# Optimization experiments

Hardware: AMD Instinct MI355X
Metric: run time of the kernel (lower is better)

The kernel has to match this reference:

```python
import jax, jax.numpy as jnp
import numpy as np

B, T, C, HS = 512, 256, 384, 64

def setup_inputs() -> dict:
    key = jax.random.key(0)
    kx, kq, kk, kv = jax.random.split(key, 4)
    x = jax.random.normal(kx, (B, T, C), dtype=jnp.float32)
    Wq = jax.random.normal(kq, (C, HS), dtype=jnp.float32) * (C ** -0.5)
    Wk = jax.random.normal(kk, (C, HS), dtype=jnp.float32) * (C ** -0.5)
    Wv = jax.random.normal(kv, (C, HS), dtype=jnp.float32) * (C ** -0.5)
    return {"x": x, "Wq": Wq, "Wk": Wk, "Wv": Wv}

def reference(x, Wq, Wk, Wv):
    # single-head causal self-attention (dropout = identity in eval mode)
    q = jnp.einsum('btc,ch->bth', x, Wq)   # [B,T,HS]
    k = jnp.einsum('btc,ch->bth', x, Wk)   # [B,T,HS]
    v = jnp.einsum('btc,ch->bth', x, Wv)   # [B,T,HS]
    scale = k.shape[-1] ** -0.5
    wei = jnp.einsum('bqh,bkh->bqk', q, k) * scale  # [B,T,T]
    causal = jnp.tril(jnp.ones((T, T), dtype=bool))
    wei = jnp.where(causal, wei, -jnp.inf)
    wei = jax.nn.softmax(wei, axis=-1)
    out = jnp.einsum('bqk,bkh->bqh', wei, v)  # [B,T,HS]
    return out
```

## Files before the change

### kernel.cpp

```cpp
#include <hip/hip_runtime.h>


typedef float f32x4 __attribute__((ext_vector_type(4)));
typedef __bf16 bf16x8 __attribute__((ext_vector_type(8)));

constexpr int T_ = 256;
constexpr int C_ = 384;
constexpr int HS_ = 64;

__device__ __forceinline__ short f2bs(float v) {
  __bf16 b = (__bf16)v;
  return __builtin_bit_cast(short, b);
}

__device__ __forceinline__ f32x4 mfma16(bf16x8 a, bf16x8 b, f32x4 c) {
  return __builtin_amdgcn_mfma_f32_16x16x32_bf16(a, b, c, 0, 0, 0);
}

__global__ void prep_wt_kernel(const float* __restrict__ Wq,
                               const float* __restrict__ Wk,
                               const float* __restrict__ Wv,
                               short* __restrict__ wt) {
  int idx = blockIdx.x * 256 + threadIdx.x;
  if (idx >= 192 * 384) return;
  int n = idx / 384;
  int k = idx - n * 384;
  const float* W = (n < 64) ? Wq : (n < 128) ? Wk : Wv;
  int h = n & 63;
  wt[idx] = f2bs(W[k * 64 + h]);
}

__device__ __forceinline__ int qswz(int row, int h) {
  return row * 64 + (h ^ ((row & 7) << 3));
}
__device__ __forceinline__ int vswz(int h, int tok) {
  return h * 256 + (tok ^ ((h & 7) << 3));
}

__global__ __launch_bounds__(512, 1) void fused_head(const float* __restrict__ x,
                                                     const short* __restrict__ wt,
                                                     float* __restrict__ out) {
  __shared__ __align__(16) short QS[256 * 64];
  __shared__ __align__(16) short KS[256 * 64];
  __shared__ __align__(16) short VT[64 * 256];
  __shared__ __align__(16) short PB[8][16 * 40];

  const int b = blockIdx.x;
  const int tid = threadIdx.x;
  const int w = tid >> 6;
  const int lr = tid & 15;
  const int lg = (tid & 63) >> 4;

  const float* xb = x + (size_t)b * (T_ * C_);

  f32x4 acc[2][12];
#pragma unroll
  for (int m = 0; m < 2; ++m)
#pragma unroll
    for (int nt = 0; nt < 12; ++nt) acc[m][nt] = f32x4{0.f, 0.f, 0.f, 0.f};

#pragma unroll
  for (int ks = 0; ks < 12; ++ks) {
    bf16x8 a[2];
#pragma unroll
    for (int m = 0; m < 2; ++m) {
      int row = (2 * w + m) * 16 + lr;
      const f32x4* p = reinterpret_cast<const f32x4*>(xb + row * C_ + ks * 32 + lg * 8);
      f32x4 f0 = p[0];
      f32x4 f1 = p[1];
      bf16x8 t;
      t[0] = (__bf16)f0[0]; t[1] = (__bf16)f0[1]; t[2] = (__bf16)f0[2]; t[3] = (__bf16)f0[3];
      t[4] = (__bf16)f1[0]; t[5] = (__bf16)f1[1]; t[6] = (__bf16)f1[2]; t[7] = (__bf16)f1[3];
      a[m] = t;
    }
#pragma unroll
    for (int nt = 0; nt < 12; ++nt) {
      bf16x8 bw = *reinterpret_cast<const bf16x8*>(wt + (nt * 16 + lr) * 384 + ks * 32 + lg * 8);
      acc[0][nt] = mfma16(a[0], bw, acc[0][nt]);
      acc[1][nt] = mfma16(a[1], bw, acc[1][nt]);
    }
  }

  const float QSCALE = 0.125f * 1.44269504f;
#pragma unroll
  for (int nt = 0; nt < 12; ++nt) {
    const int which = nt >> 2;
    const int hb = (nt & 3) * 16 + lr;
#pragma unroll
    for (int m = 0; m < 2; ++m) {
      const int rbase = (2 * w + m) * 16 + lg * 4;
#pragma unroll
      for (int j = 0; j < 4; ++j) {
        int row = rbase + j;
        float v = acc[m][nt][j];
        if (which == 0)      QS[qswz(row, hb)] = f2bs(v * QSCALE);
        else if (which == 1) KS[qswz(row, hb)] = f2bs(v);
        else                 VT[vswz(hb, row)] = f2bs(v);
      }
    }
  }

  __syncthreads();

  for (int pass = 0; pass < 2; ++pass) {
    const int t = pass ? (15 - w) : w;
    const int qrow = t * 16 + lr;
    bf16x8 aq0 = *reinterpret_cast<const bf16x8*>(&QS[qswz(qrow, lg * 8)]);
    bf16x8 aq1 = *reinterpret_cast<const bf16x8*>(&QS[qswz(qrow, 32 + lg * 8)]);

    f32x4 o[4];
    float mrun[4], lrun[4];
#pragma unroll
    for (int nt = 0; nt < 4; ++nt) o[nt] = f32x4{0.f, 0.f, 0.f, 0.f};
#pragma unroll
    for (int j = 0; j < 4; ++j) { mrun[j] = -1e30f; lrun[j] = 0.f; }

    const int nkt = (t >> 1) + 1;
    for (int kt = 0; kt < nkt; ++kt) {
      f32x4 s0 = f32x4{0.f, 0.f, 0.f, 0.f};
      f32x4 s1 = f32x4{0.f, 0.f, 0.f, 0.f};
      {
        int kr0 = kt * 32 + lr;
        int kr1 = kr0 + 16;
        bf16x8 b00 = *reinterpret_cast<const bf16x8*>(&KS[qswz(kr0, lg * 8)]);
        bf16x8 b01 = *reinterpret_cast<const bf16x8*>(&KS[qswz(kr0, 32 + lg * 8)]);
        bf16x8 b10 = *reinterpret_cast<const bf16x8*>(&KS[qswz(kr1, lg * 8)]);
        bf16x8 b11 = *reinterpret_cast<const bf16x8*>(&KS[qswz(kr1, 32 + lg * 8)]);
        s0 = mfma16(aq0, b00, s0);
        s0 = mfma16(aq1, b01, s0);
        s1 = mfma16(aq0, b10, s1);
        s1 = mfma16(aq1, b11, s1);
      }

      if (kt == nkt - 1) {
#pragma unroll
        for (int j = 0; j < 4; ++j) {
          int row = t * 16 + lg * 4 + j;
          if (kt * 32 + lr > row)      s0[j] = -1e30f;
          if (kt * 32 + 16 + lr > row) s1[j] = -1e30f;
        }
      }

      float alpha[4];
#pragma unroll
      for (int j = 0; j < 4; ++j) {
        float mx = fmaxf(s0[j], s1[j]);
        mx = fmaxf(mx, __shfl_xor(mx, 1));
        mx = fmaxf(mx, __shfl_xor(mx, 2));
        mx = fmaxf(mx, __shfl_xor(mx, 4));
        mx = fmaxf(mx, __shfl_xor(mx, 8));
        float mnew = fmaxf(mrun[j], mx);
        float al = exp2f(mrun[j] - mnew);
        mrun[j] = mnew;
        alpha[j] = al;
        float e0 = exp2f(s0[j] - mnew);
        float e1 = exp2f(s1[j] - mnew);
        float rs = e0 + e1;
        rs += __shfl_xor(rs, 1);
        rs += __shfl_xor(rs, 2);
        rs += __shfl_xor(rs, 4);
        rs += __shfl_xor(rs, 8);
        lrun[j] = lrun[j] * al + rs;
        int prow = lg * 4 + j;
        PB[w][prow * 40 + lr] = f2bs(e0);
        PB[w][prow * 40 + 16 + lr] = f2bs(e1);
      }

#pragma unroll
      for (int nt = 0; nt < 4; ++nt) {
        o[nt][0] *= alpha[0];
        o[nt][1] *= alpha[1];
        o[nt][2] *= alpha[2];
        o[nt][3] *= alpha[3];
      }
      bf16x8 ap = *reinterpret_cast<const bf16x8*>(&PB[w][lr * 40 + lg * 8]);
#pragma unroll
      for (int nt = 0; nt < 4; ++nt) {
        int h = nt * 16 + lr;
        bf16x8 bv = *reinterpret_cast<const bf16x8*>(&VT[vswz(h, kt * 32 + lg * 8)]);
        o[nt] = mfma16(ap, bv, o[nt]);
      }
    }

    float inv[4];
#pragma unroll
    for (int j = 0; j < 4; ++j) inv[j] = 1.0f / lrun[j];
    float* ob = out + ((size_t)b * T_ + t * 16 + lg * 4) * HS_;
#pragma unroll
    for (int nt = 0; nt < 4; ++nt)
#pragma unroll
      for (int j = 0; j < 4; ++j)
        ob[j * HS_ + nt * 16 + lr] = o[nt][j] * inv[j];
  }
}

extern "C" void kernel_launch(void* const* d_in, const int* in_sizes, int n_in,
                              void* d_out, int out_size, void* d_ws, size_t ws_size,
                              hipStream_t stream) {
  const float* x = (const float*)d_in[0];
  const float* Wq = (const float*)d_in[1];
  const float* Wk = (const float*)d_in[2];
  const float* Wv = (const float*)d_in[3];
  float* out = (float*)d_out;
  short* wt = (short*)d_ws;

  prep_wt_kernel<<<288, 256, 0, stream>>>(Wq, Wk, Wv, wt);
  fused_head<<<512, 512, 0, stream>>>(x, wt, out);
}
```

Before: 359.4 us.

## Split fused attention into QKV projection and attention kernels via workspace

Replaces the single fused kernel with a QKV projection kernel (1024 blocks, double-buffered weight tiles loaded into LDS with global_load_lds, x prefetched into registers) that writes swizzled bf16 Q, K and V^T to workspace. A separate attention kernel then loads K and V^T straight into LDS and reads Q from global. Splitting the work is meant to raise occupancy and overlap loads with MFMA, since the fused kernel ran one 512-thread block per CU with serialized global loads. The cost is an extra round trip of Q/K/V through global memory and a dependence on workspace size, with the old fused kernel kept as a fallback.

```diff
diff --git a/kernel.cpp b/kernel.cpp
--- a/kernel.cpp
+++ b/kernel.cpp
@@ -3,10 +3,12 @@
 
 typedef float f32x4 __attribute__((ext_vector_type(4)));
 typedef __bf16 bf16x8 __attribute__((ext_vector_type(8)));
+typedef short s16x8 __attribute__((ext_vector_type(8)));
 
 constexpr int T_ = 256;
 constexpr int C_ = 384;
 constexpr int HS_ = 64;
+constexpr int QKVE = 512 * 256 * 64;
 
 __device__ __forceinline__ short f2bs(float v) {
   __bf16 b = (__bf16)v;
@@ -15,6 +17,12 @@
 
 __device__ __forceinline__ f32x4 mfma16(bf16x8 a, bf16x8 b, f32x4 c) {
   return __builtin_amdgcn_mfma_f32_16x16x32_bf16(a, b, c, 0, 0, 0);
+}
+
+__device__ __forceinline__ void gl_lds16(const short* g, short* l) {
+  __builtin_amdgcn_global_load_lds((const __attribute__((address_space(1))) void*)g,
+                                   (__attribute__((address_space(3))) void*)l,
+                                   16, 0, 0);
 }
 
 __global__ void prep_wt_kernel(const float* __restrict__ Wq,
@@ -30,83 +38,158 @@
   wt[idx] = f2bs(W[k * 64 + h]);
 }
 
-__device__ __forceinline__ int qswz(int row, int h) {
-  return row * 64 + (h ^ ((row & 7) << 3));
-}
-__device__ __forceinline__ int vswz(int h, int tok) {
-  return h * 256 + (tok ^ ((h & 7) << 3));
-}
-
-__global__ __launch_bounds__(512, 1) void fused_head(const float* __restrict__ x,
-                                                     const short* __restrict__ wt,
-                                                     float* __restrict__ out) {
-  __shared__ __align__(16) short QS[256 * 64];
+__global__ __launch_bounds__(256, 3) void qkv_proj(const float* __restrict__ x,
+                                                   const short* __restrict__ wt,
+                                                   short* __restrict__ ws) {
+  __shared__ __align__(16) short wtile[2][4 * 192 * 8];
+  __shared__ __align__(16) short vbuf[128][65];
+
+  short* qg = ws;
+  short* kg = ws + QKVE;
+  short* vtg = ws + 2 * QKVE;
+
+  const int blk = blockIdx.x;
+  const int b = blk >> 1;
+  const int rowbase = (blk & 1) * 128;
+  const int tid = threadIdx.x;
+  const int w = tid >> 6;
+  const int lane = tid & 63;
+  const int lr = tid & 15;
+  const int lg = lane >> 4;
+
+  const float* xb = x + (size_t)b * (T_ * C_);
+
+  auto stage = [&](int buf, int ks) {
+#pragma unroll
+    for (int i = 0; i < 3; ++i) {
+      int c = i * 256 + w * 64 + lane;
+      int n = c % 192;
+      int lgc = c / 192;
+      const short* src = wt + n * 384 + ks * 32 + lgc * 8;
+      short* dst = &wtile[buf][(i * 256 + w * 64) * 8];
+      gl_lds16(src, dst);
+    }
+  };
+
+  f32x4 xf[2][2], xn[2][2];
+  auto loadx = [&](f32x4 dst[2][2], int ks) {
+#pragma unroll
+    for (int m = 0; m < 2; ++m) {
+      int row = rowbase + (2 * w + m) * 16 + lr;
+      const f32x4* p = reinterpret_cast<const f32x4*>(xb + (size_t)row * C_ + ks * 32 + lg * 8);
+      dst[m][0] = p[0];
+      dst[m][1] = p[1];
+    }
+  };
+
+  f32x4 acc[2][12];
+#pragma unroll
+  for (int m = 0; m < 2; ++m)
+#pragma unroll
+    for (int nt = 0; nt < 12; ++nt) acc[m][nt] = f32x4{0.f, 0.f, 0.f, 0.f};
+
+  stage(0, 0);
+  loadx(xf, 0);
+  __syncthreads();
+
+  for (int ks = 0; ks < 12; ++ks) {
+    const int cur = ks & 1;
+    if (ks < 11) {
+      stage(cur ^ 1, ks + 1);
+      loadx(xn, ks + 1);
+    }
+    bf16x8 a[2];
+#pragma unroll
+    for (int m = 0; m < 2; ++m) {
+      bf16x8 t;
+      t[0] = (__bf16)xf[m][0][0]; t[1] = (__bf16)xf[m][0][1];
+      t[2] = (__bf16)xf[m][0][2]; t[3] = (__bf16)xf[m][0][3];
+      t[4] = (__bf16)xf[m][1][0]; t[5] = (__bf16)xf[m][1][1];
+      t[6] = (__bf16)xf[m][1][2]; t[7] = (__bf16)xf[m][1][3];
+      a[m] = t;
+    }
+#pragma unroll
+    for (int nt = 0; nt < 12; ++nt) {
+      bf16x8 bw = *reinterpret_cast<const bf16x8*>(&wtile[cur][(lg * 192 + nt * 16 + lr) * 8]);
+      acc[0][nt] = mfma16(a[0], bw, acc[0][nt]);
+      acc[1][nt] = mfma16(a[1], bw, acc[1][nt]);
+    }
+    __syncthreads();
+    if (ks < 11) {
+#pragma unroll
+      for (int m = 0; m < 2; ++m) {
+        xf[m][0] = xn[m][0];
+        xf[m][1] = xn[m][1];
+      }
+    }
+  }
+
+  const float QSCALE = 0.125f * 1.44269504f;
+#pragma unroll
+  for (int nt = 0; nt < 12; ++nt) {
+    const int which = nt >> 2;
+    const int hb = (nt & 3) * 16 + lr;
+#pragma unroll
+    for (int m = 0; m < 2; ++m) {
+#pragma unroll
+      for (int j = 0; j < 4; ++j) {
+        int t = rowbase + (2 * w + m) * 16 + lg * 4 + j;
+        float v = acc[m][nt][j];
+        if (which == 0) {
+          qg[(size_t)b * 16384 + t * 64 + hb] = f2bs(v * QSCALE);
+        } else if (which == 1) {
+          kg[(size_t)b * 16384 + t * 64 + (hb ^ ((t & 7) << 3))] = f2bs(v);
+        } else {
+          vbuf[t - rowbase][hb] = f2bs(v);
+        }
+      }
+    }
+  }
+  __syncthreads();
+
+#pragma unroll
+  for (int r = 0; r < 4; ++r) {
+    int c = r * 256 + tid;
+    int h = c >> 4;
+    int i = c & 15;
+    s16x8 tv;
+#pragma unroll
+    for (int j = 0; j < 8; ++j) tv[j] = vbuf[i * 8 + j][h];
+    int tokbase = (rowbase + i * 8) ^ ((h & 7) << 3);
+    *reinterpret_cast<s16x8*>(vtg + (size_t)b * 16384 + h * 256 + tokbase) = tv;
+  }
+}
+
+__global__ __launch_bounds__(512, 4) void attn(const short* __restrict__ ws,
+                                               float* __restrict__ out) {
   __shared__ __align__(16) short KS[256 * 64];
   __shared__ __align__(16) short VT[64 * 256];
   __shared__ __align__(16) short PB[8][16 * 40];
 
+  const short* qg = ws;
+  const short* kg = ws + QKVE;
+  const short* vtg = ws + 2 * QKVE;
+
   const int b = blockIdx.x;
   const int tid = threadIdx.x;
   const int w = tid >> 6;
+  const int lane = tid & 63;
   const int lr = tid & 15;
-  const int lg = (tid & 63) >> 4;
-
-  const float* xb = x + (size_t)b * (T_ * C_);
-
-  f32x4 acc[2][12];
-#pragma unroll
-  for (int m = 0; m < 2; ++m)
-#pragma unroll
-    for (int nt = 0; nt < 12; ++nt) acc[m][nt] = f32x4{0.f, 0.f, 0.f, 0.f};
-
-#pragma unroll
-  for (int ks = 0; ks < 12; ++ks) {
-    bf16x8 a[2];
-#pragma unroll
-    for (int m = 0; m < 2; ++m) {
-      int row = (2 * w + m) * 16 + lr;
-      const f32x4* p = reinterpret_cast<const f32x4*>(xb + row * C_ + ks * 32 + lg * 8);
-      f32x4 f0 = p[0];
-      f32x4 f1 = p[1];
-      bf16x8 t;
-      t[0] = (__bf16)f0[0]; t[1] = (__bf16)f0[1]; t[2] = (__bf16)f0[2]; t[3] = (__bf16)f0[3];
-      t[4] = (__bf16)f1[0]; t[5] = (__bf16)f1[1]; t[6] = (__bf16)f1[2]; t[7] = (__bf16)f1[3];
-      a[m] = t;
-    }
-#pragma unroll
-    for (int nt = 0; nt < 12; ++nt) {
-      bf16x8 bw = *reinterpret_cast<const bf16x8*>(wt + (nt * 16 + lr) * 384 + ks * 32 + lg * 8);
-      acc[0][nt] = mfma16(a[0], bw, acc[0][nt]);
-      acc[1][nt] = mfma16(a[1], bw, acc[1][nt]);
-    }
-  }
-
-  const float QSCALE = 0.125f * 1.44269504f;
-#pragma unroll
-  for (int nt = 0; nt < 12; ++nt) {
-    const int which = nt >> 2;
-    const int hb = (nt & 3) * 16 + lr;
-#pragma unroll
-    for (int m = 0; m < 2; ++m) {
-      const int rbase = (2 * w + m) * 16 + lg * 4;
-#pragma unroll
-      for (int j = 0; j < 4; ++j) {
-        int row = rbase + j;
-        float v = acc[m][nt][j];
-        if (which == 0)      QS[qswz(row, hb)] = f2bs(v * QSCALE);
-        else if (which == 1) KS[qswz(row, hb)] = f2bs(v);
-        else                 VT[vswz(hb, row)] = f2bs(v);
-      }
-    }
-  }
-
+  const int lg = lane >> 4;
+
+#pragma unroll
+  for (int i = 0; i < 4; ++i) {
+    int ch = w * 4 + i;
+    gl_lds16(kg + (size_t)b * 16384 + ch * 512 + lane * 8, &KS[ch * 512]);
+    gl_lds16(vtg + (size_t)b * 16384 + ch * 512 + lane * 8, &VT[ch * 512]);
+  }
   __syncthreads();
 
   for (int pass = 0; pass < 2; ++pass) {
     const int t = pass ? (15 - w) : w;
-    const int qrow = t * 16 + lr;
-    bf16x8 aq0 = *reinterpret_cast<const bf16x8*>(&QS[qswz(qrow, lg * 8)]);
-    bf16x8 aq1 = *reinterpret_cast<const bf16x8*>(&QS[qswz(qrow, 32 + lg * 8)]);
+    const short* qrow = qg + (size_t)b * 16384 + (t * 16 + lr) * 64;
+    bf16x8 aq0 = *reinterpret_cast<const bf16x8*>(qrow + lg * 8);
+    bf16x8 aq1 = *reinterpret_cast<const bf16x8*>(qrow + 32 + lg * 8);
 
     f32x4 o[4];
     float mrun[4], lrun[4];
@@ -122,10 +205,10 @@
       {
         int kr0 = kt * 32 + lr;
         int kr1 = kr0 + 16;
-        bf16x8 b00 = *reinterpret_cast<const bf16x8*>(&KS[qswz(kr0, lg * 8)]);
-        bf16x8 b01 = *reinterpret_cast<const bf16x8*>(&KS[qswz(kr0, 32 + lg * 8)]);
-        bf16x8 b10 = *reinterpret_cast<const bf16x8*>(&KS[qswz(kr1, lg * 8)]);
-        bf16x8 b11 = *reinterpret_cast<const bf16x8*>(&KS[qswz(kr1, 32 + lg * 8)]);
+        bf16x8 b00 = *reinterpret_cast<const bf16x8*>(&KS[kr0 * 64 + ((lg * 8) ^ ((kr0 & 7) << 3))]);
+        bf16x8 b01 = *reinterpret_cast<const bf16x8*>(&KS[kr0 * 64 + ((32 + lg * 8) ^ ((kr0 & 7) << 3))]);
+        bf16x8 b10 = *reinterpret_cast<const bf16x8*>(&KS[kr1 * 64 + ((lg * 8) ^ ((kr1 & 7) << 3))]);
+        bf16x8 b11 = *reinterpret_cast<const bf16x8*>(&KS[kr1 * 64 + ((32 + lg * 8) ^ ((kr1 & 7) << 3))]);
         s0 = mfma16(aq0, b00, s0);
         s0 = mfma16(aq1, b01, s0);
         s1 = mfma16(aq0, b10, s1);
@@ -177,6 +260,170 @@
 #pragma unroll
       for (int nt = 0; nt < 4; ++nt) {
         int h = nt * 16 + lr;
+        bf16x8 bv = *reinterpret_cast<const bf16x8*>(&VT[h * 256 + ((kt * 32 + lg * 8) ^ ((h & 7) << 3))]);
+        o[nt] = mfma16(ap, bv, o[nt]);
+      }
+    }
+
+    float inv[4];
+#pragma unroll
+    for (int j = 0; j < 4; ++j) inv[j] = 1.0f / lrun[j];
+    float* ob = out + ((size_t)b * T_ + t * 16 + lg * 4) * HS_;
+#pragma unroll
+    for (int nt = 0; nt < 4; ++nt)
+#pragma unroll
+      for (int j = 0; j < 4; ++j)
+        ob[j * HS_ + nt * 16 + lr] = o[nt][j] * inv[j];
+  }
+}
+
+__device__ __forceinline__ int qswz(int row, int h) {
+  return row * 64 + (h ^ ((row & 7) << 3));
+}
+__device__ __forceinline__ int vswz(int h, int tok) {
+  return h * 256 + (tok ^ ((h & 7) << 3));
+}
+
+__global__ __launch_bounds__(512, 1) void fused_head(const float* __restrict__ x,
+                                                     const short* __restrict__ wt,
+                                                     float* __restrict__ out) {
+  __shared__ __align__(16) short QS[256 * 64];
+  __shared__ __align__(16) short KS[256 * 64];
+  __shared__ __align__(16) short VT[64 * 256];
+  __shared__ __align__(16) short PB[8][16 * 40];
+
+  const int b = blockIdx.x;
+  const int tid = threadIdx.x;
+  const int w = tid >> 6;
+  const int lr = tid & 15;
+  const int lg = (tid & 63) >> 4;
+
+  const float* xb = x + (size_t)b * (T_ * C_);
+
+  f32x4 acc[2][12];
+#pragma unroll
+  for (int m = 0; m < 2; ++m)
+#pragma unroll
+    for (int nt = 0; nt < 12; ++nt) acc[m][nt] = f32x4{0.f, 0.f, 0.f, 0.f};
+
+#pragma unroll
+  for (int ks = 0; ks < 12; ++ks) {
+    bf16x8 a[2];
+#pragma unroll
+    for (int m = 0; m < 2; ++m) {
+      int row = (2 * w + m) * 16 + lr;
+      const f32x4* p = reinterpret_cast<const f32x4*>(xb + row * C_ + ks * 32 + lg * 8);
+      f32x4 f0 = p[0];
+      f32x4 f1 = p[1];
+      bf16x8 t;
+      t[0] = (__bf16)f0[0]; t[1] = (__bf16)f0[1]; t[2] = (__bf16)f0[2]; t[3] = (__bf16)f0[3];
+      t[4] = (__bf16)f1[0]; t[5] = (__bf16)f1[1]; t[6] = (__bf16)f1[2]; t[7] = (__bf16)f1[3];
+      a[m] = t;
+    }
+#pragma unroll
+    for (int nt = 0; nt < 12; ++nt) {
+      bf16x8 bw = *reinterpret_cast<const bf16x8*>(wt + (nt * 16 + lr) * 384 + ks * 32 + lg * 8);
+      acc[0][nt] = mfma16(a[0], bw, acc[0][nt]);
+      acc[1][nt] = mfma16(a[1], bw, acc[1][nt]);
+    }
+  }
+
+  const float QSCALE = 0.125f * 1.44269504f;
+#pragma unroll
+  for (int nt = 0; nt < 12; ++nt) {
+    const int which = nt >> 2;
+    const int hb = (nt & 3) * 16 + lr;
+#pragma unroll
+    for (int m = 0; m < 2; ++m) {
+      const int rbase = (2 * w + m) * 16 + lg * 4;
+#pragma unroll
+      for (int j = 0; j < 4; ++j) {
+        int row = rbase + j;
+        float v = acc[m][nt][j];
+        if (which == 0)      QS[qswz(row, hb)] = f2bs(v * QSCALE);
+        else if (which == 1) KS[qswz(row, hb)] = f2bs(v);
+        else                 VT[vswz(hb, row)] = f2bs(v);
+      }
+    }
+  }
+
+  __syncthreads();
+
+  for (int pass = 0; pass < 2; ++pass) {
+    const int t = pass ? (15 - w) : w;
+    const int qrow = t * 16 + lr;
+    bf16x8 aq0 = *reinterpret_cast<const bf16x8*>(&QS[qswz(qrow, lg * 8)]);
+    bf16x8 aq1 = *reinterpret_cast<const bf16x8*>(&QS[qswz(qrow, 32 + lg * 8)]);
+
+    f32x4 o[4];
+    float mrun[4], lrun[4];
+#pragma unroll
+    for (int nt = 0; nt < 4; ++nt) o[nt] = f32x4{0.f, 0.f, 0.f, 0.f};
+#pragma unroll
+    for (int j = 0; j < 4; ++j) { mrun[j] = -1e30f; lrun[j] = 0.f; }
+
+    const int nkt = (t >> 1) + 1;
+    for (int kt = 0; kt < nkt; ++kt) {
+      f32x4 s0 = f32x4{0.f, 0.f, 0.f, 0.f};
+      f32x4 s1 = f32x4{0.f, 0.f, 0.f, 0.f};
+      {
+        int kr0 = kt * 32 + lr;
+        int kr1 = kr0 + 16;
+        bf16x8 b00 = *reinterpret_cast<const bf16x8*>(&KS[qswz(kr0, lg * 8)]);
+        bf16x8 b01 = *reinterpret_cast<const bf16x8*>(&KS[qswz(kr0, 32 + lg * 8)]);
+        bf16x8 b10 = *reinterpret_cast<const bf16x8*>(&KS[qswz(kr1, lg * 8)]);
+        bf16x8 b11 = *reinterpret_cast<const bf16x8*>(&KS[qswz(kr1, 32 + lg * 8)]);
+        s0 = mfma16(aq0, b00, s0);
+        s0 = mfma16(aq1, b01, s0);
+        s1 = mfma16(aq0, b10, s1);
+        s1 = mfma16(aq1, b11, s1);
+      }
+
+      if (kt == nkt - 1) {
+#pragma unroll
+        for (int j = 0; j < 4; ++j) {
+          int row = t * 16 + lg * 4 + j;
+          if (kt * 32 + lr > row)      s0[j] = -1e30f;
+          if (kt * 32 + 16 + lr > row) s1[j] = -1e30f;
+        }
+      }
+
+      float alpha[4];
+#pragma unroll
+      for (int j = 0; j < 4; ++j) {
+        float mx = fmaxf(s0[j], s1[j]);
+        mx = fmaxf(mx, __shfl_xor(mx, 1));
+        mx = fmaxf(mx, __shfl_xor(mx, 2));
+        mx = fmaxf(mx, __shfl_xor(mx, 4));
+        mx = fmaxf(mx, __shfl_xor(mx, 8));
+        float mnew = fmaxf(mrun[j], mx);
+        float al = exp2f(mrun[j] - mnew);
+        mrun[j] = mnew;
+        alpha[j] = al;
+        float e0 = exp2f(s0[j] - mnew);
+        float e1 = exp2f(s1[j] - mnew);
+        float rs = e0 + e1;
+        rs += __shfl_xor(rs, 1);
+        rs += __shfl_xor(rs, 2);
+        rs += __shfl_xor(rs, 4);
+        rs += __shfl_xor(rs, 8);
+        lrun[j] = lrun[j] * al + rs;
+        int prow = lg * 4 + j;
+        PB[w][prow * 40 + lr] = f2bs(e0);
+        PB[w][prow * 40 + 16 + lr] = f2bs(e1);
+      }
+
+#pragma unroll
+      for (int nt = 0; nt < 4; ++nt) {
+        o[nt][0] *= alpha[0];
+        o[nt][1] *= alpha[1];
+        o[nt][2] *= alpha[2];
+        o[nt][3] *= alpha[3];
+      }
+      bf16x8 ap = *reinterpret_cast<const bf16x8*>(&PB[w][lr * 40 + lg * 8]);
+#pragma unroll
+      for (int nt = 0; nt < 4; ++nt) {
+        int h = nt * 16 + lr;
         bf16x8 bv = *reinterpret_cast<const bf16x8*>(&VT[vswz(h, kt * 32 + lg * 8)]);
         o[nt] = mfma16(ap, bv, o[nt]);
       }
@@ -202,8 +449,18 @@
   const float* Wk = (const float*)d_in[2];
   const float* Wv = (const float*)d_in[3];
   float* out = (float*)d_out;
-  short* wt = (short*)d_ws;
-
-  prep_wt_kernel<<<288, 256, 0, stream>>>(Wq, Wk, Wv, wt);
-  fused_head<<<512, 512, 0, stream>>>(x, wt, out);
-}
+  short* ws = (short*)d_ws;
+
+  const size_t need = ((size_t)3 * QKVE + 192 * 384) * sizeof(short);
+
+  if (ws_size >= need) {
+    short* wt = ws + 3 * QKVE;
+    prep_wt_kernel<<<288, 256, 0, stream>>>(Wq, Wk, Wv, wt);
+    qkv_proj<<<1024, 256, 0, stream>>>(x, wt, ws);
+    attn<<<512, 512, 0, stream>>>(ws, out);
+  } else {
+    short* wt = ws;
+    prep_wt_kernel<<<288, 256, 0, stream>>>(Wq, Wk, Wv, wt);
+    fused_head<<<512, 512, 0, stream>>>(x, wt, out);
+  }
+}
```

Result: slower. 368.1 us (+2.4%).
